# Optimization experiments

Hardware: AMD Instinct MI355X
Metric: run time of the kernel (lower is better)

The kernel has to match this reference:

```python
import jax, jax.numpy as jnp
import numpy as np

B, W, L = 512, 64, 3
NODE_DIM = 172
EDGE_DIM = 172
TIME_DIM = NODE_DIM
HID = 64
EVENT_DIM = EDGE_DIM + TIME_DIM + 3  # 347
MLP_DIM = HID + 12                   # 76, if_cat=True
N_NODES = 10000
N_EDGES = 200000


def _lin_init(key, out_d, in_d):
    kw, kb = jax.random.split(key)
    s = 1.0 / np.sqrt(in_d)
    w = jax.random.uniform(kw, (out_d, in_d), minval=-s, maxval=s, dtype=jnp.float32)
    b = jax.random.uniform(kb, (out_d,), minval=-s, maxval=s, dtype=jnp.float32)
    return w, b


def setup_inputs() -> dict:
    key = jax.random.key(0)
    ks = jax.random.split(key, 24)
    inp = {}
    inp["node_idx"] = jax.random.randint(ks[0], (B, W, 2 * L), 0, N_NODES)
    inp["edge_idx"] = jax.random.randint(ks[1], (B, W, L), 0, N_EDGES)
    inp["cat_feat"] = jax.random.randint(ks[2], (B, W, 1), 0, 12)
    inp["t_records"] = jax.random.uniform(ks[3], (B, W, L), dtype=jnp.float32)
    inp["edge_identify"] = jax.random.uniform(ks[4], (B, W, L, 3), dtype=jnp.float32)
    inp["cut_time_l"] = jax.random.uniform(ks[5], (B,), dtype=jnp.float32)
    # learned tables / params
    inp["node_embed"] = jax.random.normal(ks[6], (N_NODES, NODE_DIM), dtype=jnp.float32)
    inp["edge_embed"] = jax.random.normal(ks[7], (N_EDGES, EDGE_DIM), dtype=jnp.float32)
    inp["basis_freq"] = (1.0 / 10 ** np.linspace(0, 9, TIME_DIM)).astype(np.float32)
    inp["phase"] = jnp.zeros((TIME_DIM,), dtype=jnp.float32)
    inp["lin_event_w"], inp["lin_event_b"] = _lin_init(ks[8], NODE_DIM, EVENT_DIM)
    inp["gcn_w1"], inp["gcn_b1"] = _lin_init(ks[9], HID, NODE_DIM)
    inp["gcn_w2"], inp["gcn_b2"] = _lin_init(ks[10], HID, HID)
    D2 = 2 * HID
    inp["att_w1_w"], inp["att_w1_b"] = _lin_init(ks[11], D2, D2)
    inp["att_w2_w"], _ = _lin_init(ks[12], D2, D2)
    inp["att_w2_b"] = jnp.full((D2,), 0.1, dtype=jnp.float32)
    inp["att_m1_w"], inp["att_m1_b"] = _lin_init(ks[13], HID, D2)
    inp["att_m2_w"], inp["att_m2_b"] = _lin_init(ks[14], HID, HID)
    inp["mlp_w1"], inp["mlp_b1"] = _lin_init(ks[15], MLP_DIM, MLP_DIM)
    inp["mlp_w2"], inp["mlp_b2"] = _lin_init(ks[16], HID, MLP_DIM)
    inp["mlp_w3"], inp["mlp_b3"] = _lin_init(ks[17], 1, HID)
    return inp


def _linear(x, w, b):
    return x @ w.T + b


def reference(node_idx, edge_idx, cat_feat, t_records, edge_identify, cut_time_l,
              node_embed, edge_embed, basis_freq, phase,
              lin_event_w, lin_event_b, gcn_w1, gcn_b1, gcn_w2, gcn_b2,
              att_w1_w, att_w1_b, att_w2_w, att_w2_b,
              att_m1_w, att_m1_b, att_m2_w, att_m2_b,
              mlp_w1, mlp_b1, mlp_w2, mlp_b2, mlp_w3, mlp_b3):
    # --- retrieve features (pure gathers: memory-bound) ---
    edge_f = edge_embed[edge_idx]                      # [B,W,L,E]
    delta_t = t_records[..., -1:] - t_records          # [B,W,L]
    time_f = jnp.cos(delta_t[..., None] * basis_freq + phase)  # [B,W,L,T]
    event_f = jnp.concatenate([edge_f, edge_identify, time_f], axis=-1)  # [B,W,L,EVENT_DIM]
    src_f = node_embed[node_idx[:, :, 0::2]]           # [B,W,L,NODE_DIM]
    tgt_f = node_embed[node_idx[:, :, 1::2]]

    # --- EventGCN (GINEConv-like), applied twice with src/tgt swapped ---
    event = _linear(event_f, lin_event_w, lin_event_b)  # [B,W,L,NODE_DIM]

    def gine(s, t):
        msg = jax.nn.relu(t + event)
        h = jax.nn.relu(_linear(s + msg, gcn_w1, gcn_b1))
        return _linear(h, gcn_w2, gcn_b2)               # [B,W,L,HID]

    feat = jnp.concatenate([gine(src_f, tgt_f), gine(tgt_f, src_f)], axis=-1)  # [B,W,L,2H]

    # --- walk attention (query = step 2, keys = steps 0,1) ---
    src = feat[:, :, 2:3, :]                           # [B,W,1,2H]
    tgt = feat[:, :, 0:2, :]                           # [B,W,2,2H]
    Wp = _linear(src, att_w1_w, att_w1_b)
    Wq = _linear(tgt, att_w2_w, att_w2_b)
    scores = jnp.einsum('bwqd,bwkd->bwqk', Wp, Wq)     # [B,W,1,2]
    alpha = jax.nn.softmax(scores, axis=-1)
    out = src + jnp.einsum('bwqk,bwkd->bwqd', alpha, Wq)
    h = _linear(jax.nn.relu(_linear(out, att_m1_w, att_m1_b)), att_m2_w, att_m2_b)
    src_feature = h[:, :, 0, :]                        # [B,W,HID]

    # --- category one-hot (event level) + final MLP + sigmoid ---
    cat_oh = jax.nn.one_hot(cat_feat[..., 0], 12, dtype=src_feature.dtype)  # [B,W,12]
    x = jnp.concatenate([src_feature, cat_oh], axis=-1)                      # [B,W,MLP_DIM]
    h1 = jax.nn.relu(_linear(x, mlp_w1, mlp_b1))       # dropout is identity at eval
    h2 = jax.nn.relu(_linear(h1, mlp_w2, mlp_b2))
    z = _linear(h2, mlp_w3, mlp_b3)                    # [B,W,1]
    return jax.nn.sigmoid(z)
```

## Files before the change

### kernel.cpp

```cpp
#include <hip/hip_runtime.h>
#include <hip/hip_bf16.h>
#include <math.h>

#define NW    32768
#define G     8
#define NBLK  (NW / G)
#define NT    256

#define ND    172
#define EVD   347
#define HID   64
#define D2    128
#define MLPD  76

#define W1OFF  0
#define G1OFF  (121 * 512)
#define G2OFF  (145 * 512)
#define ATTOFF (153 * 512)
#define NFRAG  217
#define WSF_BYTE_OFF 222208
#define M1OFF4 0
#define M2OFF4 2048
#define W1OFF4 3072
#define W2OFF4 4672
#define NF4    5952

#define B_EF    0
#define B_U     0
#define B_EV    9600
#define B_H     19200
#define B_FEATB 0
#define B_SRCF  6528
#define B_PQ    10624
#define B_SC    0
#define LDS_BYTES 26112

#define EFS 360
#define EVS 200
#define US  200
#define HS  72
#define FBS 136
#define SCS 204

typedef __attribute__((ext_vector_type(8))) short bf16x8;
typedef __attribute__((ext_vector_type(4))) float f32x4;

static __device__ __forceinline__ float dot4(float acc, const float4 a, const float4 b) {
  acc = fmaf(a.x, b.x, acc);
  acc = fmaf(a.y, b.y, acc);
  acc = fmaf(a.z, b.z, acc);
  acc = fmaf(a.w, b.w, acc);
  return acc;
}

static __device__ __forceinline__ short f2bf(float f) {
  union { __hip_bfloat16 h; short s; } u;
  u.h = __float2bfloat16(f);
  return u.s;
}
static __device__ __forceinline__ float bf2f(short s) {
  union { float f; unsigned u; } u;
  u.u = ((unsigned)(unsigned short)s) << 16;
  return u.f;
}

static __device__ __forceinline__ int rowmap48(int m) {
  return (m < 24) ? m : (m < 32) ? 23 : (m < 56) ? (m - 8) : 47;
}

__global__ __launch_bounds__(256) void prep_weights(
    const float* __restrict__ w1, const float* __restrict__ g1,
    const float* __restrict__ g2, const float* __restrict__ a1,
    const float* __restrict__ a2, short* __restrict__ ws)
{
  const int t = blockIdx.x * 256 + threadIdx.x;
  if (t >= NFRAG * 64) return;
  const int fid  = t >> 6;
  const int lane = t & 63;
  const int q = lane >> 4, mr = lane & 15;
  bf16x8 o;
  if (fid < 121) {
    const int nt = fid / 11, ks = fid - 11 * nt;
    const int n = nt * 16 + mr, k0 = ks * 32 + q * 8;
#pragma unroll
    for (int j = 0; j < 8; ++j) {
      const int k = k0 + j;
      o[j] = (n < ND && k < EVD) ? f2bf(w1[n * EVD + k]) : (short)0;
    }
  } else if (fid < 145) {
    const int f = fid - 121, nt = f / 6, ks = f - 6 * nt;
    const int n = nt * 16 + mr, k0 = ks * 32 + q * 8;
#pragma unroll
    for (int j = 0; j < 8; ++j) {
      const int k = k0 + j;
      o[j] = (k < ND) ? f2bf(g1[n * ND + k]) : (short)0;
    }
  } else if (fid < 153) {
    const int f = fid - 145, nt = f / 2, ks = f - 2 * nt;
    const int n = nt * 16 + mr, k0 = ks * 32 + q * 8;
#pragma unroll
    for (int j = 0; j < 8; ++j) o[j] = f2bf(g2[n * HID + k0 + j]);
  } else {
    const int f = fid - 153, nt = f / 4, ks = f - 4 * nt;
    const int n = nt * 16 + mr, k0 = ks * 32 + q * 8;
    const float* src = (n < D2) ? (a1 + n * D2) : (a2 + (n - D2) * D2);
#pragma unroll
    for (int j = 0; j < 8; ++j) o[j] = f2bf(src[k0 + j]);
  }
  *(bf16x8*)&ws[(long)t * 8] = o;
}

__global__ __launch_bounds__(256) void prep_wf(
    const float* __restrict__ m1, const float* __restrict__ m2,
    const float* __restrict__ w1, const float* __restrict__ w2,
    float4* __restrict__ wf)
{
  const int t = blockIdx.x * 256 + threadIdx.x;
  if (t >= NF4) return;
  float4 o; o.x = 0.f; o.y = 0.f; o.z = 0.f; o.w = 0.f;
  if (t < M2OFF4) {
    const int kb = t >> 6, n = t & 63;
    const float* s = m1 + n * D2 + kb * 4;
    o.x = s[0]; o.y = s[1]; o.z = s[2]; o.w = s[3];
  } else if (t < W1OFF4) {
    const int u = t - M2OFF4, kb = u >> 6, n = u & 63;
    const float* s = m2 + n * HID + kb * 4;
    o.x = s[0]; o.y = s[1]; o.z = s[2]; o.w = s[3];
  } else if (t < W2OFF4) {
    const int u = t - W1OFF4, kb = u / 80, n = u - kb * 80;
    if (n < MLPD) {
#pragma unroll
      for (int j = 0; j < 4; ++j) {
        const int k = kb * 4 + j;
        ((float*)&o)[j] = (k < MLPD) ? w1[n * MLPD + k] : 0.f;
      }
    }
  } else {
    const int u = t - W2OFF4, kb = u >> 6, n = u & 63;
#pragma unroll
    for (int j = 0; j < 4; ++j) {
      const int k = kb * 4 + j;
      ((float*)&o)[j] = (k < MLPD) ? w2[n * MLPD + k] : 0.f;
    }
  }
  wf[t] = o;
}

__global__ __launch_bounds__(256) void tempme_fused(
    const int*   __restrict__ node_idx,
    const int*   __restrict__ edge_idx,
    const int*   __restrict__ cat_feat,
    const float* __restrict__ t_records,
    const float* __restrict__ edge_identify,
    const float* __restrict__ node_embed,
    const float* __restrict__ edge_embed,
    const float* __restrict__ basis_freq,
    const float* __restrict__ phase,
    const float* __restrict__ lin_event_b,
    const float* __restrict__ gcn_b1,
    const float* __restrict__ gcn_b2,
    const float* __restrict__ att_w1_b,
    const float* __restrict__ att_w2_b,
    const float* __restrict__ att_m1_b,
    const float* __restrict__ att_m2_b,
    const float* __restrict__ mlp_b1,
    const float* __restrict__ mlp_b2,
    const float* __restrict__ mlp_w3,
    const float* __restrict__ mlp_b3,
    const short* __restrict__ ws,
    const float4* __restrict__ wsf,
    float*       __restrict__ out)
{
  __shared__ __align__(16) unsigned char smem[LDS_BYTES];
  short* EF    = (short*)&smem[B_EF];
  short* EV    = (short*)&smem[B_EV];
  short* U     = (short*)&smem[B_U];
  short* Hs    = (short*)&smem[B_H];
  short* FEATB = (short*)&smem[B_FEATB];
  float* SRCF  = (float*)&smem[B_SRCF];
  float* PQ    = (float*)&smem[B_PQ];
  float* SC    = (float*)&smem[B_SC];

  const int tid  = threadIdx.x;
  const int lane = tid & 63;
  const int wv   = tid >> 6;
  const int q    = lane >> 4;
  const int mr   = lane & 15;
  const int bw0  = blockIdx.x * G;

  int   eidx_[6], si_[6], ti_[6], rid_[6];
  float dt_[6];
#pragma unroll
  for (int i = 0; i < 6; ++i) {
    const int r = wv + 4 * i;
    const int g = r / 3;
    const int l = r - 3 * g;
    const int bw = bw0 + g;
    const int rid = bw * 3 + l;
    rid_[i]  = rid;
    eidx_[i] = edge_idx[rid];
    si_[i]   = node_idx[bw * 6 + 2 * l];
    ti_[i]   = node_idx[bw * 6 + 2 * l + 1];
    dt_[i]   = t_records[bw * 3 + 2] - t_records[rid];
  }

  float pg[6][3];
#pragma unroll
  for (int i = 0; i < 6; ++i) {
    const float* erow = edge_embed + (long)eidx_[i] * ND;
#pragma unroll
    for (int c = 0; c < 3; ++c) {
      const int k = c * 64 + lane;
      float v = 0.f;
      if (k < ND)            v = erow[k];
      else if (k < ND + 3)   v = edge_identify[rid_[i] * 3 + (k - ND)];
      pg[i][c] = v;
    }
  }

#pragma unroll
  for (int i = 0; i < 6; ++i) {
    const int r = wv + 4 * i;
    const float dt = dt_[i];
#pragma unroll
    for (int c = 0; c < 6; ++c) {
      const int k = c * 64 + lane;
      float v;
      if (c < 3) {
        v = pg[i][c];
        if (k >= ND + 3) {
          const int d = k - (ND + 3);
          v = __cosf(fmaf(dt, basis_freq[d], phase[d]));
        }
      } else {
        v = 0.f;
        if (k < EVD) {
          const int d = k - (ND + 3);
          v = __cosf(fmaf(dt, basis_freq[d], phase[d]));
        }
      }
      if (k < 352) EF[r * EFS + k] = f2bf(v);
    }
  }

  float ps[6][3], pt[6][3];
#pragma unroll
  for (int i = 0; i < 6; ++i) {
    const float* srow = node_embed + (long)si_[i] * ND;
    const float* trow = node_embed + (long)ti_[i] * ND;
#pragma unroll
    for (int c = 0; c < 3; ++c) {
      const int k = c * 64 + lane;
      float sv = 0.f, tv = 0.f;
      if (k < ND) { sv = srow[k]; tv = trow[k]; }
      ps[i][c] = sv;
      pt[i][c] = tv;
    }
  }
  __syncthreads();

  {
    const int a1r = (mr < 8) ? (16 + mr) : 23;
    const int nnt = (wv == 3) ? 2 : 3;
    f32x4 acc[3][2];
#pragma unroll
    for (int t = 0; t < 3; ++t)
#pragma unroll
      for (int mt = 0; mt < 2; ++mt) acc[t][mt] = (f32x4){0.f, 0.f, 0.f, 0.f};

#pragma unroll 2
    for (int ks = 0; ks < 11; ++ks) {
      const int k0 = ks * 32 + q * 8;
      const bf16x8 a0 = *(const bf16x8*)&EF[mr * EFS + k0];
      const bf16x8 a1 = *(const bf16x8*)&EF[a1r * EFS + k0];
#pragma unroll 1
      for (int t = 0; t < nnt; ++t) {
        const int nt = wv + 4 * t;
        const bf16x8 b = *(const bf16x8*)&ws[W1OFF + ((nt * 11 + ks) * 64 + lane) * 8];
        acc[t][0] = __builtin_amdgcn_mfma_f32_16x16x32_bf16(a0, b, acc[t][0], 0, 0, 0);
        acc[t][1] = __builtin_amdgcn_mfma_f32_16x16x32_bf16(a1, b, acc[t][1], 0, 0, 0);
      }
    }
    __syncthreads();
#pragma unroll 1
    for (int t = 0; t < nnt; ++t) {
      const int n = (wv + 4 * t) * 16 + mr;
      const float bo = (n < ND) ? lin_event_b[n] : 0.f;
#pragma unroll
      for (int mt = 0; mt < 2; ++mt)
#pragma unroll
        for (int reg = 0; reg < 4; ++reg) {
          const int m = mt * 16 + q * 4 + reg;
          if (m < 24) EV[m * EVS + n] = f2bf(acc[t][mt][reg] + bo);
        }
    }
  }
  __syncthreads();

  {
    float ev[6][3];
#pragma unroll
    for (int i = 0; i < 6; ++i) {
      const int r = wv + 4 * i;
#pragma unroll
      for (int c = 0; c < 3; ++c) {
        const int k = c * 64 + lane;
        ev[i][c] = (k < ND) ? bf2f(EV[r * EVS + k]) : 0.f;
      }
    }
#pragma unroll
    for (int i = 0; i < 6; ++i) {
      const int r = wv + 4 * i;
#pragma unroll
      for (int c = 0; c < 3; ++c) {
        const int k = c * 64 + lane;
        float u0v = 0.f, u1v = 0.f;
        if (k < ND) {
          const float e = ev[i][c];
          const float s = ps[i][c];
          const float t = pt[i][c];
          u0v = s + fmaxf(t + e, 0.f);
          u1v = t + fmaxf(s + e, 0.f);
        }
        U[r * US + k]        = f2bf(u0v);
        U[(24 + r) * US + k] = f2bf(u1v);
      }
    }
  }
  __syncthreads();

  {
    const int urow = rowmap48(wv * 16 + mr);
    f32x4 acc[4];
#pragma unroll
    for (int nt = 0; nt < 4; ++nt) acc[nt] = (f32x4){0.f, 0.f, 0.f, 0.f};
#pragma unroll 2
    for (int ks = 0; ks < 6; ++ks) {
      const int k0 = ks * 32 + q * 8;
      const bf16x8 a = *(const bf16x8*)&U[urow * US + k0];
#pragma unroll 1
      for (int nt = 0; nt < 4; ++nt) {
        const bf16x8 b = *(const bf16x8*)&ws[G1OFF + ((nt * 6 + ks) * 64 + lane) * 8];
        acc[nt] = __builtin_amdgcn_mfma_f32_16x16x32_bf16(a, b, acc[nt], 0, 0, 0);
      }
    }
#pragma unroll 1
    for (int nt = 0; nt < 4; ++nt) {
      const int j = nt * 16 + mr;
      const float b1 = gcn_b1[j];
#pragma unroll
      for (int reg = 0; reg < 4; ++reg) {
        const int m = wv * 16 + q * 4 + reg;
        int hr = -1;
        if (m < 24) hr = m;
        else if (m >= 32 && m < 56) hr = m - 8;
        if (hr >= 0) Hs[hr * HS + j] = f2bf(fmaxf(acc[nt][reg] + b1, 0.f));
      }
    }
  }
  __syncthreads();

  {
    const int hrow = rowmap48(wv * 16 + mr);
    f32x4 acc[4];
#pragma unroll
    for (int nt = 0; nt < 4; ++nt) acc[nt] = (f32x4){0.f, 0.f, 0.f, 0.f};
#pragma unroll
    for (int ks = 0; ks < 2; ++ks) {
      const int k0 = ks * 32 + q * 8;
      const bf16x8 a = *(const bf16x8*)&Hs[hrow * HS + k0];
#pragma unroll 1
      for (int nt = 0; nt < 4; ++nt) {
        const bf16x8 b = *(const bf16x8*)&ws[G2OFF + ((nt * 2 + ks) * 64 + lane) * 8];
        acc[nt] = __builtin_amdgcn_mfma_f32_16x16x32_bf16(a, b, acc[nt], 0, 0, 0);
      }
    }
#pragma unroll 1
    for (int nt = 0; nt < 4; ++nt) {
      const int j = nt * 16 + mr;
      const float b2 = gcn_b2[j];
#pragma unroll
      for (int reg = 0; reg < 4; ++reg) {
        const int m = wv * 16 + q * 4 + reg;
        int d = -1, r = 0;
        if (m < 24) { d = 0; r = m; }
        else if (m >= 32 && m < 56) { d = 1; r = m - 32; }
        if (d >= 0) {
          const float v = acc[nt][reg] + b2;
          const int n = d * HID + j;
          FEATB[r * FBS + n] = f2bf(v);
          if (r % 3 == 2) SRCF[(r / 3) * 128 + n] = v;
        }
      }
    }
  }
  __syncthreads();

  {
    const int fr1 = (16 + mr < 24) ? (16 + mr) : 23;
    f32x4 acc[4][2];
#pragma unroll
    for (int tt = 0; tt < 4; ++tt)
#pragma unroll
      for (int mt = 0; mt < 2; ++mt) acc[tt][mt] = (f32x4){0.f, 0.f, 0.f, 0.f};
#pragma unroll 2
    for (int ks = 0; ks < 4; ++ks) {
      const int k0 = ks * 32 + q * 8;
      const bf16x8 a0 = *(const bf16x8*)&FEATB[mr * FBS + k0];
      const bf16x8 a1 = *(const bf16x8*)&FEATB[fr1 * FBS + k0];
#pragma unroll 1
      for (int tt = 0; tt < 4; ++tt) {
        const int nt = wv * 4 + tt;
        const bf16x8 b = *(const bf16x8*)&ws[ATTOFF + ((nt * 4 + ks) * 64 + lane) * 8];
        acc[tt][0] = __builtin_amdgcn_mfma_f32_16x16x32_bf16(a0, b, acc[tt][0], 0, 0, 0);
        acc[tt][1] = __builtin_amdgcn_mfma_f32_16x16x32_bf16(a1, b, acc[tt][1], 0, 0, 0);
      }
    }
#pragma unroll 1
    for (int tt = 0; tt < 4; ++tt) {
      const int n = (wv * 4 + tt) * 16 + mr;
      const float bias = (n < D2) ? att_w1_b[n] : att_w2_b[n - D2];
#pragma unroll
      for (int mt = 0; mt < 2; ++mt)
#pragma unroll
        for (int reg = 0; reg < 4; ++reg) {
          const int m = mt * 16 + q * 4 + reg;
          if (m < 24) {
            const int l = m % 3;
            if (l == 2) { if (n < D2)  PQ[m * 128 + n]        = acc[tt][mt][reg] + bias; }
            else        { if (n >= D2) PQ[m * 128 + (n - D2)] = acc[tt][mt][reg] + bias; }
          }
        }
    }
  }
  __syncthreads();

  {
    const int ga = wv * 2, gb = ga + 1;
    float* A_a = SC + ga * SCS;  float* Bb_a = A_a + 128;
    float* A_b = SC + gb * SCS;  float* Bb_b = A_b + 128;

#pragma unroll 1
    for (int it = 0; it < 2; ++it) {
      const int g = ga + it;
      float* Ao = SC + g * SCS;
      const float p0  = PQ[(3 * g + 2) * 128 + lane];
      const float p1  = PQ[(3 * g + 2) * 128 + 64 + lane];
      const float q00 = PQ[(3 * g + 0) * 128 + lane];
      const float q01 = PQ[(3 * g + 0) * 128 + 64 + lane];
      const float q10 = PQ[(3 * g + 1) * 128 + lane];
      const float q11 = PQ[(3 * g + 1) * 128 + 64 + lane];
      float s0 = p0 * q00 + p1 * q01;
      float s1 = p0 * q10 + p1 * q11;
#pragma unroll
      for (int off = 32; off >= 1; off >>= 1) {
        s0 += __shfl_xor(s0, off, 64);
        s1 += __shfl_xor(s1, off, 64);
      }
      const float mx = fmaxf(s0, s1);
      const float e0 = __expf(s0 - mx), e1 = __expf(s1 - mx);
      const float inv = 1.f / (e0 + e1);
      const float a0 = e0 * inv, a1 = e1 * inv;
      Ao[lane]      = SRCF[g * 128 + lane]      + a0 * q00 + a1 * q10;
      Ao[64 + lane] = SRCF[g * 128 + 64 + lane] + a0 * q01 + a1 * q11;
    }

    const float4* M1P = wsf + M1OFF4;
    const float4* M2P = wsf + M2OFF4;
    const float4* W1P = wsf + W1OFF4;
    const float4* W2P = wsf + W2OFF4;

    {
      float aa0 = 0.f, aa1 = 0.f, bb0 = 0.f, bb1 = 0.f;
#pragma unroll 4
      for (int kb = 0; kb < 32; kb += 2) {
        const float4 w0 = M1P[kb * 64 + lane];
        const float4 w1 = M1P[(kb + 1) * 64 + lane];
        const float4 xa0 = *(const float4*)&A_a[kb * 4];
        const float4 xa1 = *(const float4*)&A_a[kb * 4 + 4];
        const float4 xb0 = *(const float4*)&A_b[kb * 4];
        const float4 xb1 = *(const float4*)&A_b[kb * 4 + 4];
        aa0 = dot4(aa0, w0, xa0); aa1 = dot4(aa1, w1, xa1);
        bb0 = dot4(bb0, w0, xb0); bb1 = dot4(bb1, w1, xb1);
      }
      const float bi = att_m1_b[lane];
      Bb_a[lane] = fmaxf(bi + aa0 + aa1, 0.f);
      Bb_b[lane] = fmaxf(bi + bb0 + bb1, 0.f);
    }

    float hv_a, hv_b;
    {
      float aa0 = 0.f, aa1 = 0.f, bb0 = 0.f, bb1 = 0.f;
#pragma unroll 4
      for (int kb = 0; kb < 16; kb += 2) {
        const float4 w0 = M2P[kb * 64 + lane];
        const float4 w1 = M2P[(kb + 1) * 64 + lane];
        const float4 xa0 = *(const float4*)&Bb_a[kb * 4];
        const float4 xa1 = *(const float4*)&Bb_a[kb * 4 + 4];
        const float4 xb0 = *(const float4*)&Bb_b[kb * 4];
        const float4 xb1 = *(const float4*)&Bb_b[kb * 4 + 4];
        aa0 = dot4(aa0, w0, xa0); aa1 = dot4(aa1, w1, xa1);
        bb0 = dot4(bb0, w0, xb0); bb1 = dot4(bb1, w1, xb1);
      }
      const float bi = att_m2_b[lane];
      hv_a = bi + aa0 + aa1;
      hv_b = bi + bb0 + bb1;
    }

    A_a[lane] = hv_a;
    A_b[lane] = hv_b;
    if (lane < 16) {
      const int ca = cat_feat[bw0 + ga];
      const int cb = cat_feat[bw0 + gb];
      A_a[64 + lane] = (lane < 12 && ca == lane) ? 1.f : 0.f;
      A_b[64 + lane] = (lane < 12 && cb == lane) ? 1.f : 0.f;
    }

    {
      float an = 0.f, an2 = 0.f, bn = 0.f, bn2 = 0.f;
      const int l2 = 64 + (lane & 15);
#pragma unroll 4
      for (int kb = 0; kb < 20; ++kb) {
        const float4 wn  = W1P[kb * 80 + lane];
        const float4 wn2 = W1P[kb * 80 + l2];
        const float4 xa = *(const float4*)&A_a[kb * 4];
        const float4 xb = *(const float4*)&A_b[kb * 4];
        an  = dot4(an,  wn,  xa); an2 = dot4(an2, wn2, xa);
        bn  = dot4(bn,  wn,  xb); bn2 = dot4(bn2, wn2, xb);
      }
      const float b1n = mlp_b1[lane];
      Bb_a[lane] = fmaxf(b1n + an, 0.f);
      Bb_b[lane] = fmaxf(b1n + bn, 0.f);
      if (lane < 12) {
        const float b1n2 = mlp_b1[64 + lane];
        Bb_a[64 + lane] = fmaxf(b1n2 + an2, 0.f);
        Bb_b[64 + lane] = fmaxf(b1n2 + bn2, 0.f);
      }
    }

    {
      float ha = 0.f, hb = 0.f;
#pragma unroll 4
      for (int kb = 0; kb < 20; ++kb) {
        const float4 w  = W2P[kb * 64 + lane];
        const float4 xa = *(const float4*)&Bb_a[kb * 4];
        const float4 xb = *(const float4*)&Bb_b[kb * 4];
        ha = dot4(ha, w, xa);
        hb = dot4(hb, w, xb);
      }
      const float b2 = mlp_b2[lane];
      const float h2a = fmaxf(b2 + ha, 0.f);
      const float h2b = fmaxf(b2 + hb, 0.f);
      const float w3 = mlp_w3[lane];
      float za = w3 * h2a, zb = w3 * h2b;
#pragma unroll
      for (int off = 32; off >= 1; off >>= 1) {
        za += __shfl_xor(za, off, 64);
        zb += __shfl_xor(zb, off, 64);
      }
      if (lane == 0) {
        const float b3 = mlp_b3[0];
        out[bw0 + ga] = 1.f / (1.f + __expf(-(za + b3)));
        out[bw0 + gb] = 1.f / (1.f + __expf(-(zb + b3)));
      }
    }
  }
}

extern "C" void kernel_launch(void* const* d_in, const int* in_sizes, int n_in,
                              void* d_out, int out_size, void* d_ws, size_t ws_size,
                              hipStream_t stream) {
  short* ws = (short*)d_ws;
  float4* wsf = (float4*)((char*)d_ws + WSF_BYTE_OFF);
  prep_weights<<<(NFRAG * 64 + 255) / 256, 256, 0, stream>>>(
      (const float*)d_in[10],
      (const float*)d_in[12],
      (const float*)d_in[14],
      (const float*)d_in[16],
      (const float*)d_in[18],
      ws);
  prep_wf<<<(NF4 + 255) / 256, 256, 0, stream>>>(
      (const float*)d_in[20],
      (const float*)d_in[22],
      (const float*)d_in[24],
      (const float*)d_in[26],
      wsf);
  tempme_fused<<<NBLK, NT, 0, stream>>>(
      (const int*)d_in[0],
      (const int*)d_in[1],
      (const int*)d_in[2],
      (const float*)d_in[3],
      (const float*)d_in[4],
      (const float*)d_in[6],
      (const float*)d_in[7],
      (const float*)d_in[8],
      (const float*)d_in[9],
      (const float*)d_in[11],
      (const float*)d_in[13],
      (const float*)d_in[15],
      (const float*)d_in[17],
      (const float*)d_in[19],
      (const float*)d_in[21],
      (const float*)d_in[23],
      (const float*)d_in[25],
      (const float*)d_in[27],
      (const float*)d_in[28],
      (const float*)d_in[29],
      ws, wsf,
      (float*)d_out);
}
```

Before: 481.4 us.

## Double block to 512 threads and redistribute MFMA tiles across eight waves

Each block now runs eight wavefronts instead of four, and every stage is repartitioned. Gather rows, event-linear N tiles, GCN M×N tile pairs, attention N tiles and per-walk MLP tails are now split three, one or two per wave instead of six, three, four or two. The GCN stages drop the padded 48-row remap (M tiles of 64) and run only three real M tiles, cutting wasted MFMA work. The aim is shorter per-wave critical paths and more memory-level parallelism per block. The cost is higher register and occupancy pressure under launch_bounds(512,8) and uneven work across waves.

After: 570.3 us. +18.5%, slower.

```diff
diff --git a/kernel.cpp b/kernel.cpp
--- a/kernel.cpp
+++ b/kernel.cpp
@@ -5,7 +5,7 @@
 #define NW    32768
 #define G     8
 #define NBLK  (NW / G)
-#define NT    256
+#define NT    512
 
 #define ND    172
 #define EVD   347
@@ -62,10 +62,6 @@
   union { float f; unsigned u; } u;
   u.u = ((unsigned)(unsigned short)s) << 16;
   return u.f;
-}
-
-static __device__ __forceinline__ int rowmap48(int m) {
-  return (m < 24) ? m : (m < 32) ? 23 : (m < 56) ? (m - 8) : 47;
 }
 
 __global__ __launch_bounds__(256) void prep_weights(
@@ -146,7 +142,7 @@
   wf[t] = o;
 }
 
-__global__ __launch_bounds__(256) void tempme_fused(
+__global__ __launch_bounds__(512, 8) void tempme_fused(
     const int*   __restrict__ node_idx,
     const int*   __restrict__ edge_idx,
     const int*   __restrict__ cat_feat,
@@ -188,11 +184,11 @@
   const int mr   = lane & 15;
   const int bw0  = blockIdx.x * G;
 
-  int   eidx_[6], si_[6], ti_[6], rid_[6];
-  float dt_[6];
-#pragma unroll
-  for (int i = 0; i < 6; ++i) {
-    const int r = wv + 4 * i;
+  int   eidx_[3], si_[3], ti_[3], rid_[3];
+  float dt_[3];
+#pragma unroll
+  for (int i = 0; i < 3; ++i) {
+    const int r = wv + 8 * i;
     const int g = r / 3;
     const int l = r - 3 * g;
     const int bw = bw0 + g;
@@ -204,9 +200,9 @@
     dt_[i]   = t_records[bw * 3 + 2] - t_records[rid];
   }
 
-  float pg[6][3];
-#pragma unroll
-  for (int i = 0; i < 6; ++i) {
+  float pg[3][3];
+#pragma unroll
+  for (int i = 0; i < 3; ++i) {
     const float* erow = edge_embed + (long)eidx_[i] * ND;
 #pragma unroll
     for (int c = 0; c < 3; ++c) {
@@ -219,8 +215,8 @@
   }
 
 #pragma unroll
-  for (int i = 0; i < 6; ++i) {
-    const int r = wv + 4 * i;
+  for (int i = 0; i < 3; ++i) {
+    const int r = wv + 8 * i;
     const float dt = dt_[i];
 #pragma unroll
     for (int c = 0; c < 6; ++c) {
@@ -243,9 +239,9 @@
     }
   }
 
-  float ps[6][3], pt[6][3];
-#pragma unroll
-  for (int i = 0; i < 6; ++i) {
+  float ps[3][3], pt[3][3];
+#pragma unroll
+  for (int i = 0; i < 3; ++i) {
     const float* srow = node_embed + (long)si_[i] * ND;
     const float* trow = node_embed + (long)ti_[i] * ND;
 #pragma unroll
@@ -261,10 +257,10 @@
 
   {
     const int a1r = (mr < 8) ? (16 + mr) : 23;
-    const int nnt = (wv == 3) ? 2 : 3;
-    f32x4 acc[3][2];
-#pragma unroll
-    for (int t = 0; t < 3; ++t)
+    const int nnt = (wv < 3) ? 2 : 1;
+    f32x4 acc[2][2];
+#pragma unroll
+    for (int t = 0; t < 2; ++t)
 #pragma unroll
       for (int mt = 0; mt < 2; ++mt) acc[t][mt] = (f32x4){0.f, 0.f, 0.f, 0.f};
 
@@ -275,7 +271,7 @@
       const bf16x8 a1 = *(const bf16x8*)&EF[a1r * EFS + k0];
 #pragma unroll 1
       for (int t = 0; t < nnt; ++t) {
-        const int nt = wv + 4 * t;
+        const int nt = wv + 8 * t;
         const bf16x8 b = *(const bf16x8*)&ws[W1OFF + ((nt * 11 + ks) * 64 + lane) * 8];
         acc[t][0] = __builtin_amdgcn_mfma_f32_16x16x32_bf16(a0, b, acc[t][0], 0, 0, 0);
         acc[t][1] = __builtin_amdgcn_mfma_f32_16x16x32_bf16(a1, b, acc[t][1], 0, 0, 0);
@@ -284,7 +280,7 @@
     __syncthreads();
 #pragma unroll 1
     for (int t = 0; t < nnt; ++t) {
-      const int n = (wv + 4 * t) * 16 + mr;
+      const int n = (wv + 8 * t) * 16 + mr;
       const float bo = (n < ND) ? lin_event_b[n] : 0.f;
 #pragma unroll
       for (int mt = 0; mt < 2; ++mt)
@@ -298,10 +294,10 @@
   __syncthreads();
 
   {
-    float ev[6][3];
-#pragma unroll
-    for (int i = 0; i < 6; ++i) {
-      const int r = wv + 4 * i;
+    float ev[3][3];
+#pragma unroll
+    for (int i = 0; i < 3; ++i) {
+      const int r = wv + 8 * i;
 #pragma unroll
       for (int c = 0; c < 3; ++c) {
         const int k = c * 64 + lane;
@@ -309,8 +305,8 @@
       }
     }
 #pragma unroll
-    for (int i = 0; i < 6; ++i) {
-      const int r = wv + 4 * i;
+    for (int i = 0; i < 3; ++i) {
+      const int r = wv + 8 * i;
 #pragma unroll
       for (int c = 0; c < 3; ++c) {
         const int k = c * 64 + lane;
@@ -330,67 +326,57 @@
   __syncthreads();
 
   {
-    const int urow = rowmap48(wv * 16 + mr);
-    f32x4 acc[4];
-#pragma unroll
-    for (int nt = 0; nt < 4; ++nt) acc[nt] = (f32x4){0.f, 0.f, 0.f, 0.f};
+    const int np = (wv < 4) ? 2 : 1;
+#pragma unroll 1
+    for (int pp = 0; pp < np; ++pp) {
+      const int p = wv + 8 * pp;
+      const int mtile = p >> 2, ntb = p & 3;
+      const int urow = mtile * 16 + mr;
+      f32x4 acc = (f32x4){0.f, 0.f, 0.f, 0.f};
 #pragma unroll 2
-    for (int ks = 0; ks < 6; ++ks) {
-      const int k0 = ks * 32 + q * 8;
-      const bf16x8 a = *(const bf16x8*)&U[urow * US + k0];
+      for (int ks = 0; ks < 6; ++ks) {
+        const int k0 = ks * 32 + q * 8;
+        const bf16x8 a = *(const bf16x8*)&U[urow * US + k0];
+        const bf16x8 b = *(const bf16x8*)&ws[G1OFF + ((ntb * 6 + ks) * 64 + lane) * 8];
+        acc = __builtin_amdgcn_mfma_f32_16x16x32_bf16(a, b, acc, 0, 0, 0);
+      }
+      const int j = ntb * 16 + mr;
+      const float b1 = gcn_b1[j];
+#pragma unroll
+      for (int reg = 0; reg < 4; ++reg) {
+        const int m = mtile * 16 + q * 4 + reg;
+        Hs[m * HS + j] = f2bf(fmaxf(acc[reg] + b1, 0.f));
+      }
+    }
+  }
+  __syncthreads();
+
+  {
+    const int np = (wv < 4) ? 2 : 1;
 #pragma unroll 1
-      for (int nt = 0; nt < 4; ++nt) {
-        const bf16x8 b = *(const bf16x8*)&ws[G1OFF + ((nt * 6 + ks) * 64 + lane) * 8];
-        acc[nt] = __builtin_amdgcn_mfma_f32_16x16x32_bf16(a, b, acc[nt], 0, 0, 0);
-      }
-    }
-#pragma unroll 1
-    for (int nt = 0; nt < 4; ++nt) {
-      const int j = nt * 16 + mr;
-      const float b1 = gcn_b1[j];
+    for (int pp = 0; pp < np; ++pp) {
+      const int p = wv + 8 * pp;
+      const int mtile = p >> 2, ntb = p & 3;
+      const int hrow = mtile * 16 + mr;
+      f32x4 acc = (f32x4){0.f, 0.f, 0.f, 0.f};
+#pragma unroll
+      for (int ks = 0; ks < 2; ++ks) {
+        const int k0 = ks * 32 + q * 8;
+        const bf16x8 a = *(const bf16x8*)&Hs[hrow * HS + k0];
+        const bf16x8 b = *(const bf16x8*)&ws[G2OFF + ((ntb * 2 + ks) * 64 + lane) * 8];
+        acc = __builtin_amdgcn_mfma_f32_16x16x32_bf16(a, b, acc, 0, 0, 0);
+      }
+      const int j = ntb * 16 + mr;
+      const float b2 = gcn_b2[j];
 #pragma unroll
       for (int reg = 0; reg < 4; ++reg) {
-        const int m = wv * 16 + q * 4 + reg;
-        int hr = -1;
-        if (m < 24) hr = m;
-        else if (m >= 32 && m < 56) hr = m - 8;
-        if (hr >= 0) Hs[hr * HS + j] = f2bf(fmaxf(acc[nt][reg] + b1, 0.f));
-      }
-    }
-  }
-  __syncthreads();
-
-  {
-    const int hrow = rowmap48(wv * 16 + mr);
-    f32x4 acc[4];
-#pragma unroll
-    for (int nt = 0; nt < 4; ++nt) acc[nt] = (f32x4){0.f, 0.f, 0.f, 0.f};
-#pragma unroll
-    for (int ks = 0; ks < 2; ++ks) {
-      const int k0 = ks * 32 + q * 8;
-      const bf16x8 a = *(const bf16x8*)&Hs[hrow * HS + k0];
-#pragma unroll 1
-      for (int nt = 0; nt < 4; ++nt) {
-        const bf16x8 b = *(const bf16x8*)&ws[G2OFF + ((nt * 2 + ks) * 64 + lane) * 8];
-        acc[nt] = __builtin_amdgcn_mfma_f32_16x16x32_bf16(a, b, acc[nt], 0, 0, 0);
-      }
-    }
-#pragma unroll 1
-    for (int nt = 0; nt < 4; ++nt) {
-      const int j = nt * 16 + mr;
-      const float b2 = gcn_b2[j];
-#pragma unroll
-      for (int reg = 0; reg < 4; ++reg) {
-        const int m = wv * 16 + q * 4 + reg;
-        int d = -1, r = 0;
-        if (m < 24) { d = 0; r = m; }
-        else if (m >= 32 && m < 56) { d = 1; r = m - 32; }
-        if (d >= 0) {
-          const float v = acc[nt][reg] + b2;
-          const int n = d * HID + j;
-          FEATB[r * FBS + n] = f2bf(v);
-          if (r % 3 == 2) SRCF[(r / 3) * 128 + n] = v;
-        }
+        const int m = mtile * 16 + q * 4 + reg;
+        const int d = (m < 24) ? 0 : 1;
+        const int r = m - 24 * d;
+        const float v = acc[reg] + b2;
+        const int n = d * HID + j;
+        FEATB[r * FBS + n] = f2bf(v);
+        if (r % 3 == 2) SRCF[(r / 3) * 128 + n] = v;
       }
     }
   }
@@ -398,9 +384,9 @@
 
   {
     const int fr1 = (16 + mr < 24) ? (16 + mr) : 23;
-    f32x4 acc[4][2];
-#pragma unroll
-    for (int tt = 0; tt < 4; ++tt)
+    f32x4 acc[2][2];
+#pragma unroll
+    for (int tt = 0; tt < 2; ++tt)
 #pragma unroll
       for (int mt = 0; mt < 2; ++mt) acc[tt][mt] = (f32x4){0.f, 0.f, 0.f, 0.f};
 #pragma unroll 2
@@ -409,16 +395,16 @@
       const bf16x8 a0 = *(const bf16x8*)&FEATB[mr * FBS + k0];
       const bf16x8 a1 = *(const bf16x8*)&FEATB[fr1 * FBS + k0];
 #pragma unroll 1
-      for (int tt = 0; tt < 4; ++tt) {
-        const int nt = wv * 4 + tt;
+      for (int tt = 0; tt < 2; ++tt) {
+        const int nt = wv * 2 + tt;
         const bf16x8 b = *(const bf16x8*)&ws[ATTOFF + ((nt * 4 + ks) * 64 + lane) * 8];
         acc[tt][0] = __builtin_amdgcn_mfma_f32_16x16x32_bf16(a0, b, acc[tt][0], 0, 0, 0);
         acc[tt][1] = __builtin_amdgcn_mfma_f32_16x16x32_bf16(a1, b, acc[tt][1], 0, 0, 0);
       }
     }
 #pragma unroll 1
-    for (int tt = 0; tt < 4; ++tt) {
-      const int n = (wv * 4 + tt) * 16 + mr;
+    for (int tt = 0; tt < 2; ++tt) {
+      const int n = (wv * 2 + tt) * 16 + mr;
       const float bias = (n < D2) ? att_w1_b[n] : att_w2_b[n - D2];
 #pragma unroll
       for (int mt = 0; mt < 2; ++mt)
@@ -436,14 +422,11 @@
   __syncthreads();
 
   {
-    const int ga = wv * 2, gb = ga + 1;
-    float* A_a = SC + ga * SCS;  float* Bb_a = A_a + 128;
-    float* A_b = SC + gb * SCS;  float* Bb_b = A_b + 128;
-
-#pragma unroll 1
-    for (int it = 0; it < 2; ++it) {
-      const int g = ga + it;
-      float* Ao = SC + g * SCS;
+    const int g = wv;
+    float* Aw = SC + g * SCS;
+    float* Bw = Aw + 128;
+
+    {
       const float p0  = PQ[(3 * g + 2) * 128 + lane];
       const float p1  = PQ[(3 * g + 2) * 128 + 64 + lane];
       const float q00 = PQ[(3 * g + 0) * 128 + lane];
@@ -461,8 +444,8 @@
       const float e0 = __expf(s0 - mx), e1 = __expf(s1 - mx);
       const float inv = 1.f / (e0 + e1);
       const float a0 = e0 * inv, a1 = e1 * inv;
-      Ao[lane]      = SRCF[g * 128 + lane]      + a0 * q00 + a1 * q10;
-      Ao[64 + lane] = SRCF[g * 128 + 64 + lane] + a0 * q01 + a1 * q11;
+      Aw[lane]      = SRCF[g * 128 + lane]      + a0 * q00 + a1 * q10;
+      Aw[64 + lane] = SRCF[g * 128 + 64 + lane] + a0 * q01 + a1 * q11;
     }
 
     const float4* M1P = wsf + M1OFF4;
@@ -471,98 +454,66 @@
     const float4* W2P = wsf + W2OFF4;
 
     {
-      float aa0 = 0.f, aa1 = 0.f, bb0 = 0.f, bb1 = 0.f;
+      float aa0 = 0.f, aa1 = 0.f;
 #pragma unroll 4
       for (int kb = 0; kb < 32; kb += 2) {
         const float4 w0 = M1P[kb * 64 + lane];
         const float4 w1 = M1P[(kb + 1) * 64 + lane];
-        const float4 xa0 = *(const float4*)&A_a[kb * 4];
-        const float4 xa1 = *(const float4*)&A_a[kb * 4 + 4];
-        const float4 xb0 = *(const float4*)&A_b[kb * 4];
-        const float4 xb1 = *(const float4*)&A_b[kb * 4 + 4];
-        aa0 = dot4(aa0, w0, xa0); aa1 = dot4(aa1, w1, xa1);
-        bb0 = dot4(bb0, w0, xb0); bb1 = dot4(bb1, w1, xb1);
-      }
-      const float bi = att_m1_b[lane];
-      Bb_a[lane] = fmaxf(bi + aa0 + aa1, 0.f);
-      Bb_b[lane] = fmaxf(bi + bb0 + bb1, 0.f);
-    }
-
-    float hv_a, hv_b;
+        const float4 x0 = *(const float4*)&Aw[kb * 4];
+        const float4 x1 = *(const float4*)&Aw[kb * 4 + 4];
+        aa0 = dot4(aa0, w0, x0); aa1 = dot4(aa1, w1, x1);
+      }
+      Bw[lane] = fmaxf(att_m1_b[lane] + aa0 + aa1, 0.f);
+    }
+
+    float hv;
     {
-      float aa0 = 0.f, aa1 = 0.f, bb0 = 0.f, bb1 = 0.f;
+      float aa0 = 0.f, aa1 = 0.f;
 #pragma unroll 4
       for (int kb = 0; kb < 16; kb += 2) {
         const float4 w0 = M2P[kb * 64 + lane];
         const float4 w1 = M2P[(kb + 1) * 64 + lane];
-        const float4 xa0 = *(const float4*)&Bb_a[kb * 4];
-        const float4 xa1 = *(const float4*)&Bb_a[kb * 4 + 4];
-        const float4 xb0 = *(const float4*)&Bb_b[kb * 4];
-        const float4 xb1 = *(const float4*)&Bb_b[kb * 4 + 4];
-        aa0 = dot4(aa0, w0, xa0); aa1 = dot4(aa1, w1, xa1);
-        bb0 = dot4(bb0, w0, xb0); bb1 = dot4(bb1, w1, xb1);
-      }
-      const float bi = att_m2_b[lane];
-      hv_a = bi + aa0 + aa1;
-      hv_b = bi + bb0 + bb1;
-    }
-
-    A_a[lane] = hv_a;
-    A_b[lane] = hv_b;
+        const float4 x0 = *(const float4*)&Bw[kb * 4];
+        const float4 x1 = *(const float4*)&Bw[kb * 4 + 4];
+        aa0 = dot4(aa0, w0, x0); aa1 = dot4(aa1, w1, x1);
+      }
+      hv = att_m2_b[lane] + aa0 + aa1;
+    }
+
+    Aw[lane] = hv;
     if (lane < 16) {
-      const int ca = cat_feat[bw0 + ga];
-      const int cb = cat_feat[bw0 + gb];
-      A_a[64 + lane] = (lane < 12 && ca == lane) ? 1.f : 0.f;
-      A_b[64 + lane] = (lane < 12 && cb == lane) ? 1.f : 0.f;
+      const int ca = cat_feat[bw0 + g];
+      Aw[64 + lane] = (lane < 12 && ca == lane) ? 1.f : 0.f;
     }
 
     {
-      float an = 0.f, an2 = 0.f, bn = 0.f, bn2 = 0.f;
+      float an = 0.f, an2 = 0.f;
       const int l2 = 64 + (lane & 15);
 #pragma unroll 4
       for (int kb = 0; kb < 20; ++kb) {
         const float4 wn  = W1P[kb * 80 + lane];
         const float4 wn2 = W1P[kb * 80 + l2];
-        const float4 xa = *(const float4*)&A_a[kb * 4];
-        const float4 xb = *(const float4*)&A_b[kb * 4];
-        an  = dot4(an,  wn,  xa); an2 = dot4(an2, wn2, xa);
-        bn  = dot4(bn,  wn,  xb); bn2 = dot4(bn2, wn2, xb);
-      }
-      const float b1n = mlp_b1[lane];
-      Bb_a[lane] = fmaxf(b1n + an, 0.f);
-      Bb_b[lane] = fmaxf(b1n + bn, 0.f);
-      if (lane < 12) {
-        const float b1n2 = mlp_b1[64 + lane];
-        Bb_a[64 + lane] = fmaxf(b1n2 + an2, 0.f);
-        Bb_b[64 + lane] = fmaxf(b1n2 + bn2, 0.f);
-      }
+        const float4 x  = *(const float4*)&Aw[kb * 4];
+        an  = dot4(an,  wn,  x);
+        an2 = dot4(an2, wn2, x);
+      }
+      Bw[lane] = fmaxf(mlp_b1[lane] + an, 0.f);
+      if (lane < 12) Bw[64 + lane] = fmaxf(mlp_b1[64 + lane] + an2, 0.f);
     }
 
     {
-      float ha = 0.f, hb = 0.f;
+      float ha = 0.f;
 #pragma unroll 4
       for (int kb = 0; kb < 20; ++kb) {
-        const float4 w  = W2P[kb * 64 + lane];
-        const float4 xa = *(const float4*)&Bb_a[kb * 4];
-        const float4 xb = *(const float4*)&Bb_b[kb * 4];
-        ha = dot4(ha, w, xa);
-        hb = dot4(hb, w, xb);
-      }
-      const float b2 = mlp_b2[lane];
-      const float h2a = fmaxf(b2 + ha, 0.f);
-      const float h2b = fmaxf(b2 + hb, 0.f);
-      const float w3 = mlp_w3[lane];
-      float za = w3 * h2a, zb = w3 * h2b;
-#pragma unroll
-      for (int off = 32; off >= 1; off >>= 1) {
-        za += __shfl_xor(za, off, 64);
-        zb += __shfl_xor(zb, off, 64);
-      }
-      if (lane == 0) {
-        const float b3 = mlp_b3[0];
-        out[bw0 + ga] = 1.f / (1.f + __expf(-(za + b3)));
-        out[bw0 + gb] = 1.f / (1.f + __expf(-(zb + b3)));
-      }
+        const float4 w = W2P[kb * 64 + lane];
+        const float4 x = *(const float4*)&Bw[kb * 4];
+        ha = dot4(ha, w, x);
+      }
+      const float h2 = fmaxf(mlp_b2[lane] + ha, 0.f);
+      float zz = mlp_w3[lane] * h2;
+#pragma unroll
+      for (int off = 32; off >= 1; off >>= 1) zz += __shfl_xor(zz, off, 64);
+      if (lane == 0) out[bw0 + g] = 1.f / (1.f + __expf(-(zz + mlp_b3[0])));
     }
   }
 }
```
